# Kernel tuning notes

Measured on AMD Instinct MI355X. Metric: run time of the kernel, lower is better.

## Reference

```python
import jax, jax.numpy as jnp
import numpy as np

N_NODES = 50000
IN_C, HID_C, OUT_C = 128, 128, 64
N_EDGES = 800000


def setup_inputs() -> dict:
    key = jax.random.key(0)
    k1, k2, k3, k4, k5, k6 = jax.random.split(key, 6)
    x = jax.random.normal(k1, (N_NODES, IN_C), dtype=jnp.float32)
    edge_index = jax.random.randint(k2, (2, N_EDGES), 0, N_NODES, dtype=jnp.int64)
    # Glorot-ish init for the two GCN layer weights + biases
    W1 = jax.random.normal(k3, (IN_C, HID_C), dtype=jnp.float32) / np.sqrt(IN_C)
    b1 = jnp.zeros((HID_C,), dtype=jnp.float32)
    W2 = jax.random.normal(k4, (HID_C, OUT_C), dtype=jnp.float32) / np.sqrt(HID_C)
    b2 = jnp.zeros((OUT_C,), dtype=jnp.float32)
    return {"x": x, "edge_index": edge_index, "W1": W1, "b1": b1, "W2": W2, "b2": b2}


def _gcn_norm(edge_index, num_nodes):
    # Add self-loops, then symmetric normalization: deg^-1/2[row] * deg^-1/2[col]
    loops = jnp.arange(num_nodes, dtype=edge_index.dtype)
    row = jnp.concatenate([edge_index[0], loops])  # target nodes
    col = jnp.concatenate([edge_index[1], loops])  # source nodes
    ones = jnp.ones(row.shape[0], dtype=jnp.float32)
    deg = jax.ops.segment_sum(ones, row, num_segments=num_nodes)
    dinv = jnp.where(deg > 0, jax.lax.rsqrt(jnp.maximum(deg, 1.0)), 0.0)
    norm = dinv[row] * dinv[col]  # [E + N]
    return row, col, norm


def _gcn_conv(x, row, col, norm, W, b, num_nodes):
    h = x @ W                              # [N, C_out] — transform first (fewer FLOPs)
    msg = h[col] * norm[:, None]           # gather + scale  [E+N, C_out]
    out = jax.ops.segment_sum(msg, row, num_segments=num_nodes)  # scatter-add
    return out + b


def reference(x, edge_index, W1, b1, W2, b2):
    n = x.shape[0]
    row, col, norm = _gcn_norm(edge_index, n)
    h = _gcn_conv(x, row, col, norm, W1, b1, n)
    # original applies x.relu() then non_linearity (ReLU()) — idempotent, one relu suffices
    h = jax.nn.relu(h)
    return _gcn_conv(h, row, col, norm, W2, b2, n)
```

## Files before the change

### kernel.cpp

```cpp
#include <hip/hip_runtime.h>


#define CHUNKS 256

typedef short bf16x8 __attribute__((ext_vector_type(8)));
typedef float f32x4 __attribute__((ext_vector_type(4)));

__device__ __forceinline__ float bf2f(unsigned int u16) {
    return __uint_as_float(u16 << 16);
}
__device__ __forceinline__ unsigned int f2bf_rne(float f) {
    unsigned int u = __float_as_uint(f);
    return (u + 0x7fffu + ((u >> 16) & 1u)) >> 16;
}
__device__ __forceinline__ unsigned int pack2bf(float a, float b) {
    return f2bf_rne(a) | (f2bf_rne(b) << 16);
}


__global__ __launch_bounds__(256) void hist_kernel(
    const int* __restrict__ row, int E, int CE, int NB, int* __restrict__ cnt)
{
    __shared__ int hist[256];
    const int c = blockIdx.x, t = threadIdx.x;
    hist[t] = 0;
    __syncthreads();
    int s = c * CE, e = min(E, s + CE);
    for (int i = s + t; i < e; i += 256) atomicAdd(&hist[row[i] >> 8], 1);
    __syncthreads();
    if (t < NB) cnt[t * CHUNKS + c] = hist[t];
}

__global__ __launch_bounds__(256) void scanA_kernel(int* __restrict__ cnt, int* __restrict__ tot)
{
    __shared__ int s[256];
    const int b = blockIdx.x, t = threadIdx.x;
    int v = cnt[b * CHUNKS + t];
    s[t] = v; __syncthreads();
    #pragma unroll
    for (int d = 1; d < 256; d <<= 1) {
        int xv = (t >= d) ? s[t - d] : 0;
        __syncthreads();
        s[t] += xv;
        __syncthreads();
    }
    cnt[b * CHUNKS + t] = s[t] - v;
    if (t == 255) tot[b] = s[255];
}

__global__ __launch_bounds__(256) void scanB_kernel(
    const int* __restrict__ tot, int* __restrict__ bstart, int NB, int E)
{
    __shared__ int s[256];
    const int t = threadIdx.x;
    int v = (t < NB) ? tot[t] : 0;
    s[t] = v; __syncthreads();
    #pragma unroll
    for (int d = 1; d < 256; d <<= 1) {
        int xv = (t >= d) ? s[t - d] : 0;
        __syncthreads();
        s[t] += xv;
        __syncthreads();
    }
    if (t < NB) bstart[t] = s[t] - v;
    if (t == 0) bstart[NB] = E;
}

__global__ __launch_bounds__(256) void scatter_kernel(
    const int* __restrict__ row, const int* __restrict__ col, int E, int CE, int NB,
    const int* __restrict__ cnt, const int* __restrict__ bstart,
    unsigned int* __restrict__ bucket)
{
    __shared__ int curL[256];
    const int c = blockIdx.x, t = threadIdx.x;
    if (t < NB) curL[t] = bstart[t] + cnt[t * CHUNKS + c];
    __syncthreads();
    int s = c * CE, e = min(E, s + CE);
    for (int i = s + t; i < e; i += 256) {
        int r = row[i];
        int b = r >> 8;
        int pos = atomicAdd(&curL[b], 1);
        bucket[pos] = (unsigned)(r & 255) | ((unsigned)col[i] << 8);
    }
}

__global__ __launch_bounds__(256) void bucketize_kernel(
    const int* __restrict__ bstart, unsigned int* __restrict__ bucket,
    float* __restrict__ dinv, int2* __restrict__ off2, int N)
{
    __shared__ unsigned int ent[8192];
    __shared__ int hist[256], scn[256], cnt2[256];
    const int b = blockIdx.x, t = threadIdx.x;
    const int n0 = b * 256;

    hist[t] = 0;
    cnt2[t] = 0;
    __syncthreads();

    const int bs = bstart[b], be = bstart[b + 1];
    const int m = min(be - bs, 8192);

    for (int i = t; i < m; i += 256) {
        unsigned int v = bucket[bs + i];
        ent[i] = v;
        atomicAdd(&hist[v & 255u], 1);
    }
    __syncthreads();

    int h = hist[t];
    scn[t] = h;
    __syncthreads();
    #pragma unroll
    for (int d = 1; d < 256; d <<= 1) {
        int xv = (t >= d) ? scn[t - d] : 0;
        __syncthreads();
        scn[t] += xv;
        __syncthreads();
    }
    int base = scn[t] - h;

    int node = n0 + t;
    if (node < N) {
        dinv[node] = rsqrtf((float)(h + 1));
        off2[node] = make_int2(bs + base, bs + base + h);
    }
    scn[t] = base;
    __syncthreads();

    for (int i = t; i < m; i += 256) {
        unsigned int v = ent[i];
        int r = v & 255u;
        int slot = atomicAdd(&cnt2[r], 1);
        bucket[bs + scn[r] + slot] = v >> 8;
    }
}


__global__ __launch_bounds__(256) void wtrans_kernel(
    const float* __restrict__ W, unsigned short* __restrict__ Wt, int C)
{
    int i = blockIdx.x * 256 + threadIdx.x;
    if (i < 128 * C) {
        int k = i / C, c = i - k * C;
        Wt[c * 128 + k] = (unsigned short)f2bf_rne(W[i]);
    }
}

template <int CT>
__global__ __launch_bounds__(256) void gemm_mfma_kernel(
    const float* __restrict__ X, const unsigned short* __restrict__ Wt,
    const float* __restrict__ dinv, unsigned short* __restrict__ out, int N)
{
    constexpr int COUT = CT * 64;
    __shared__ unsigned short As[64 * 128];
    __shared__ unsigned short Bs[COUT * 128];
    __shared__ float dl[64];

    const int t = threadIdx.x;
    const int m0 = blockIdx.x * 64;

    #pragma unroll
    for (int i = 0; i < 8; ++i) {
        int f = i * 256 + t;
        int r = f >> 5, c4 = f & 31;
        int rg = m0 + r;
        float4 v = (rg < N) ? ((const float4*)X)[(size_t)rg * 32 + c4]
                            : make_float4(0.f, 0.f, 0.f, 0.f);
        uint2 p;
        p.x = pack2bf(v.x, v.y);
        p.y = pack2bf(v.z, v.w);
        int cb = c4 * 8;
        *(uint2*)((char*)As + r * 256 + (cb ^ ((r & 7) << 4))) = p;
    }
    #pragma unroll
    for (int i = 0; i < CT * 8; ++i) {
        int f = i * 256 + t;
        int r = f >> 5;
        int cb = (f & 31) * 8;
        uint2 p = ((const uint2*)Wt)[f];
        *(uint2*)((char*)Bs + r * 256 + (cb ^ ((r & 7) << 4))) = p;
    }
    if (t < 64) dl[t] = (m0 + t < N) ? dinv[m0 + t] : 0.f;
    __syncthreads();

    const int w = t >> 6, l = t & 63;
    const int lr = l & 15, lk = l >> 4;

    bf16x8 af[4][4];
    #pragma unroll
    for (int mt = 0; mt < 4; ++mt)
        #pragma unroll
        for (int kt = 0; kt < 4; ++kt) {
            int r = mt * 16 + lr;
            int cb = kt * 64 + lk * 16;
            af[mt][kt] = *(const bf16x8*)((const char*)As + r * 256 + (cb ^ ((r & 7) << 4)));
        }
    bf16x8 bfr[CT][4];
    #pragma unroll
    for (int ct = 0; ct < CT; ++ct)
        #pragma unroll
        for (int kt = 0; kt < 4; ++kt) {
            int c = w * (CT * 16) + ct * 16 + lr;
            int cb = kt * 64 + lk * 16;
            bfr[ct][kt] = *(const bf16x8*)((const char*)Bs + c * 256 + (cb ^ ((c & 7) << 4)));
        }

    f32x4 acc[4][CT];
    #pragma unroll
    for (int mt = 0; mt < 4; ++mt)
        #pragma unroll
        for (int ct = 0; ct < CT; ++ct)
            acc[mt][ct] = f32x4{0.f, 0.f, 0.f, 0.f};

    #pragma unroll
    for (int kt = 0; kt < 4; ++kt)
        #pragma unroll
        for (int mt = 0; mt < 4; ++mt)
            #pragma unroll
            for (int ct = 0; ct < CT; ++ct)
                acc[mt][ct] = __builtin_amdgcn_mfma_f32_16x16x32_bf16(
                    af[mt][kt], bfr[ct][kt], acc[mt][ct], 0, 0, 0);

    #pragma unroll
    for (int mt = 0; mt < 4; ++mt) {
        #pragma unroll
        for (int ct = 0; ct < CT; ++ct) {
            #pragma unroll
            for (int r = 0; r < 4; ++r) {
                int rowl = mt * 16 + lk * 4 + r;
                int grow = m0 + rowl;
                if (grow < N) {
                    int c = w * (CT * 16) + ct * 16 + lr;
                    float v = acc[mt][ct][r] * dl[rowl];
                    out[(size_t)grow * COUT + c] = (unsigned short)f2bf_rne(v);
                }
            }
        }
    }
}


__global__ __launch_bounds__(64) void agg1_kernel(
    const unsigned short* __restrict__ hs, const unsigned int* __restrict__ csr,
    const int2* __restrict__ off2, const float* __restrict__ dinv,
    const float* __restrict__ bias, float* __restrict__ out, int N)
{
    const int n = blockIdx.x;
    const int ch = threadIdx.x * 2;

    unsigned int sv = *(const unsigned int*)&hs[(size_t)n * 128 + ch];
    float ax = bf2f(sv & 0xffffu), ay = bf2f(sv >> 16);

    int2 se = off2[n];
    int j = se.x, e = se.y;
    for (; j + 3 < e; j += 4) {
        int c0 = csr[j], c1 = csr[j + 1], c2 = csr[j + 2], c3 = csr[j + 3];
        unsigned int v0 = *(const unsigned int*)&hs[(size_t)c0 * 128 + ch];
        unsigned int v1 = *(const unsigned int*)&hs[(size_t)c1 * 128 + ch];
        unsigned int v2 = *(const unsigned int*)&hs[(size_t)c2 * 128 + ch];
        unsigned int v3 = *(const unsigned int*)&hs[(size_t)c3 * 128 + ch];
        ax += bf2f(v0 & 0xffffu); ay += bf2f(v0 >> 16);
        ax += bf2f(v1 & 0xffffu); ay += bf2f(v1 >> 16);
        ax += bf2f(v2 & 0xffffu); ay += bf2f(v2 >> 16);
        ax += bf2f(v3 & 0xffffu); ay += bf2f(v3 >> 16);
    }
    for (; j < e; ++j) {
        unsigned int v = *(const unsigned int*)&hs[(size_t)csr[j] * 128 + ch];
        ax += bf2f(v & 0xffffu); ay += bf2f(v >> 16);
    }

    float d = dinv[n];
    float2 b = *(const float2*)&bias[ch];
    float2 o;
    o.x = fmaxf(d * ax + b.x, 0.0f);
    o.y = fmaxf(d * ay + b.y, 0.0f);
    *(float2*)&out[(size_t)n * 128 + ch] = o;
}

__global__ __launch_bounds__(64) void agg2_kernel(
    const unsigned short* __restrict__ hs, const unsigned int* __restrict__ csr,
    const int2* __restrict__ off2, const float* __restrict__ dinv,
    const float* __restrict__ bias, float* __restrict__ out, int N)
{
    const int n = blockIdx.x;
    const int l = threadIdx.x;
    const int half = l >> 5;
    const int ch = (l & 31) * 2;

    int2 se = off2[n];
    int j = se.x, e = se.y;
    float ax = 0.f, ay = 0.f;
    for (; j + 3 < e; j += 4) {
        int c0 = csr[j + half];
        int c1 = csr[j + 2 + half];
        unsigned int v0 = *(const unsigned int*)&hs[(size_t)c0 * 64 + ch];
        unsigned int v1 = *(const unsigned int*)&hs[(size_t)c1 * 64 + ch];
        ax += bf2f(v0 & 0xffffu); ay += bf2f(v0 >> 16);
        ax += bf2f(v1 & 0xffffu); ay += bf2f(v1 >> 16);
    }
    if (j + 1 < e) {
        int c = csr[j + half];
        unsigned int v = *(const unsigned int*)&hs[(size_t)c * 64 + ch];
        ax += bf2f(v & 0xffffu); ay += bf2f(v >> 16);
        j += 2;
    }
    if (j < e && half == 0) {
        unsigned int v = *(const unsigned int*)&hs[(size_t)csr[j] * 64 + ch];
        ax += bf2f(v & 0xffffu); ay += bf2f(v >> 16);
    }

    ax += __shfl_xor(ax, 32);
    ay += __shfl_xor(ay, 32);

    if (half == 0) {
        unsigned int sv = *(const unsigned int*)&hs[(size_t)n * 64 + ch];
        ax += bf2f(sv & 0xffffu); ay += bf2f(sv >> 16);
        float d = dinv[n];
        float2 b = *(const float2*)&bias[ch];
        float2 o;
        o.x = d * ax + b.x;
        o.y = d * ay + b.y;
        *(float2*)&out[(size_t)n * 64 + ch] = o;
    }
}

extern "C" void kernel_launch(void* const* d_in, const int* in_sizes, int n_in,
                              void* d_out, int out_size, void* d_ws, size_t ws_size,
                              hipStream_t stream)
{
    const float* x  = (const float*)d_in[0];
    const int*   ei = (const int*)d_in[1];
    const float* W1 = (const float*)d_in[2];
    const float* b1 = (const float*)d_in[3];
    const float* W2 = (const float*)d_in[4];
    const float* b2 = (const float*)d_in[5];
    float* out = (float*)d_out;

    const int N = in_sizes[0] / 128;
    const int E = in_sizes[1] / 2;
    const int* row = ei;
    const int* col = ei + E;
    const int NB = (N + 255) / 256;
    const int CE = (E + CHUNKS - 1) / CHUNKS;

    char* ws = (char*)d_ws;
    size_t o = 0;
    auto take = [&](size_t bytes) { void* p = ws + o; o = (o + bytes + 255) & ~(size_t)255; return p; };
    int*   cnt    = (int*)  take((size_t)NB * CHUNKS * 4);
    int*   tot    = (int*)  take((size_t)NB * 4);
    int*   bstart = (int*)  take((size_t)(NB + 1) * 4);
    unsigned int* bucket = (unsigned int*)take((size_t)E * 4);
    float* dinv   = (float*)take((size_t)N * 4);
    int2*  off2   = (int2*) take((size_t)N * 8);
    unsigned short* Wt1 = (unsigned short*)take(128 * 128 * 2);
    unsigned short* Wt2 = (unsigned short*)take(64 * 128 * 2);
    unsigned short* hs  = (unsigned short*)take((size_t)N * 128 * 2);
    float* a1     = (float*)take((size_t)N * 128 * 4);
    unsigned short* hs2 = hs;

    hist_kernel<<<CHUNKS, 256, 0, stream>>>(row, E, CE, NB, cnt);
    scanA_kernel<<<NB, 256, 0, stream>>>(cnt, tot);
    scanB_kernel<<<1, 256, 0, stream>>>(tot, bstart, NB, E);
    scatter_kernel<<<CHUNKS, 256, 0, stream>>>(row, col, E, CE, NB, cnt, bstart, bucket);
    bucketize_kernel<<<NB, 256, 0, stream>>>(bstart, bucket, dinv, off2, N);

    wtrans_kernel<<<(128 * 128 + 255) / 256, 256, 0, stream>>>(W1, Wt1, 128);
    wtrans_kernel<<<(128 * 64 + 255) / 256, 256, 0, stream>>>(W2, Wt2, 64);

    gemm_mfma_kernel<2><<<(N + 63) / 64, 256, 0, stream>>>(x, Wt1, dinv, hs, N);
    agg1_kernel<<<N, 64, 0, stream>>>(hs, bucket, off2, dinv, b1, a1, N);

    gemm_mfma_kernel<1><<<(N + 63) / 64, 256, 0, stream>>>(a1, Wt2, dinv, hs2, N);
    agg2_kernel<<<N, 64, 0, stream>>>(hs2, bucket, off2, dinv, b2, out, N);
}
```

Baseline: 123.1 us.

## Store layer-1 activations as bf16 and widen aggregation gathers to 16-byte loads

The first aggregation now writes bf16 activations instead of fp32, which halves the a1 write and the second GEMM's read; the GEMM gains a bf16-input path. Both aggregation kernels now gather 8 channels per lane with uint4 loads and spread neighbors across lane groups, then combine the groups with shuffle reductions. This lowers the number of memory instructions per edge. The two weight-transpose launches are merged into one. The extra bf16 rounding of the intermediate activations changes numerics slightly, though the GEMM already converted that input to bf16.

```diff
diff --git a/kernel.cpp b/kernel.cpp
--- a/kernel.cpp
+++ b/kernel.cpp
@@ -15,6 +15,12 @@
 }
 __device__ __forceinline__ unsigned int pack2bf(float a, float b) {
     return f2bf_rne(a) | (f2bf_rne(b) << 16);
+}
+__device__ __forceinline__ void add8(float* acc, uint4 p) {
+    acc[0] += bf2f(p.x & 0xffffu); acc[1] += bf2f(p.x >> 16);
+    acc[2] += bf2f(p.y & 0xffffu); acc[3] += bf2f(p.y >> 16);
+    acc[4] += bf2f(p.z & 0xffffu); acc[5] += bf2f(p.z >> 16);
+    acc[6] += bf2f(p.w & 0xffffu); acc[7] += bf2f(p.w >> 16);
 }
 
 
@@ -137,18 +143,25 @@
 
 
 __global__ __launch_bounds__(256) void wtrans_kernel(
-    const float* __restrict__ W, unsigned short* __restrict__ Wt, int C)
+    const float* __restrict__ W1, const float* __restrict__ W2,
+    unsigned short* __restrict__ Wt1, unsigned short* __restrict__ Wt2)
 {
     int i = blockIdx.x * 256 + threadIdx.x;
-    if (i < 128 * C) {
-        int k = i / C, c = i - k * C;
-        Wt[c * 128 + k] = (unsigned short)f2bf_rne(W[i]);
-    }
-}
-
-template <int CT>
+    if (i < 128 * 128) {
+        int k = i >> 7, c = i & 127;
+        Wt1[c * 128 + k] = (unsigned short)f2bf_rne(W1[i]);
+    } else {
+        int j = i - 128 * 128;
+        if (j < 128 * 64) {
+            int k = j >> 6, c = j & 63;
+            Wt2[c * 128 + k] = (unsigned short)f2bf_rne(W2[j]);
+        }
+    }
+}
+
+template <int CT, bool BF16IN>
 __global__ __launch_bounds__(256) void gemm_mfma_kernel(
-    const float* __restrict__ X, const unsigned short* __restrict__ Wt,
+    const void* __restrict__ Xv, const unsigned short* __restrict__ Wt,
     const float* __restrict__ dinv, unsigned short* __restrict__ out, int N)
 {
     constexpr int COUT = CT * 64;
@@ -159,18 +172,33 @@
     const int t = threadIdx.x;
     const int m0 = blockIdx.x * 64;
 
-    #pragma unroll
-    for (int i = 0; i < 8; ++i) {
-        int f = i * 256 + t;
-        int r = f >> 5, c4 = f & 31;
-        int rg = m0 + r;
-        float4 v = (rg < N) ? ((const float4*)X)[(size_t)rg * 32 + c4]
-                            : make_float4(0.f, 0.f, 0.f, 0.f);
-        uint2 p;
-        p.x = pack2bf(v.x, v.y);
-        p.y = pack2bf(v.z, v.w);
-        int cb = c4 * 8;
-        *(uint2*)((char*)As + r * 256 + (cb ^ ((r & 7) << 4))) = p;
+    if (BF16IN) {
+        const unsigned short* X = (const unsigned short*)Xv;
+        #pragma unroll
+        for (int i = 0; i < 4; ++i) {
+            int f = i * 256 + t;
+            int r = f >> 4, c16 = f & 15;
+            int rg = m0 + r;
+            uint4 p = (rg < N) ? ((const uint4*)X)[(size_t)rg * 16 + c16]
+                               : make_uint4(0u, 0u, 0u, 0u);
+            int cb = c16 * 16;
+            *(uint4*)((char*)As + r * 256 + (cb ^ ((r & 7) << 4))) = p;
+        }
+    } else {
+        const float* X = (const float*)Xv;
+        #pragma unroll
+        for (int i = 0; i < 8; ++i) {
+            int f = i * 256 + t;
+            int r = f >> 5, c4 = f & 31;
+            int rg = m0 + r;
+            float4 v = (rg < N) ? ((const float4*)X)[(size_t)rg * 32 + c4]
+                                : make_float4(0.f, 0.f, 0.f, 0.f);
+            uint2 p;
+            p.x = pack2bf(v.x, v.y);
+            p.y = pack2bf(v.z, v.w);
+            int cb = c4 * 8;
+            *(uint2*)((char*)As + r * 256 + (cb ^ ((r & 7) << 4))) = p;
+        }
     }
     #pragma unroll
     for (int i = 0; i < CT * 8; ++i) {
@@ -243,38 +271,51 @@
 __global__ __launch_bounds__(64) void agg1_kernel(
     const unsigned short* __restrict__ hs, const unsigned int* __restrict__ csr,
     const int2* __restrict__ off2, const float* __restrict__ dinv,
-    const float* __restrict__ bias, float* __restrict__ out, int N)
+    const float* __restrict__ bias, unsigned short* __restrict__ out, int N)
 {
     const int n = blockIdx.x;
-    const int ch = threadIdx.x * 2;
-
-    unsigned int sv = *(const unsigned int*)&hs[(size_t)n * 128 + ch];
-    float ax = bf2f(sv & 0xffffu), ay = bf2f(sv >> 16);
+    const int l = threadIdx.x;
+    const int q = l & 15, g = l >> 4;
+
+    float acc[8] = {};
+    if (g == 0)
+        add8(acc, *(const uint4*)&hs[(size_t)n * 128 + q * 8]);
 
     int2 se = off2[n];
     int j = se.x, e = se.y;
-    for (; j + 3 < e; j += 4) {
-        int c0 = csr[j], c1 = csr[j + 1], c2 = csr[j + 2], c3 = csr[j + 3];
-        unsigned int v0 = *(const unsigned int*)&hs[(size_t)c0 * 128 + ch];
-        unsigned int v1 = *(const unsigned int*)&hs[(size_t)c1 * 128 + ch];
-        unsigned int v2 = *(const unsigned int*)&hs[(size_t)c2 * 128 + ch];
-        unsigned int v3 = *(const unsigned int*)&hs[(size_t)c3 * 128 + ch];
-        ax += bf2f(v0 & 0xffffu); ay += bf2f(v0 >> 16);
-        ax += bf2f(v1 & 0xffffu); ay += bf2f(v1 >> 16);
-        ax += bf2f(v2 & 0xffffu); ay += bf2f(v2 >> 16);
-        ax += bf2f(v3 & 0xffffu); ay += bf2f(v3 >> 16);
-    }
-    for (; j < e; ++j) {
-        unsigned int v = *(const unsigned int*)&hs[(size_t)csr[j] * 128 + ch];
-        ax += bf2f(v & 0xffffu); ay += bf2f(v >> 16);
-    }
-
-    float d = dinv[n];
-    float2 b = *(const float2*)&bias[ch];
-    float2 o;
-    o.x = fmaxf(d * ax + b.x, 0.0f);
-    o.y = fmaxf(d * ay + b.y, 0.0f);
-    *(float2*)&out[(size_t)n * 128 + ch] = o;
+    for (; j + 7 < e; j += 8) {
+        int c0 = csr[j + g], c1 = csr[j + 4 + g];
+        uint4 p0 = *(const uint4*)&hs[(size_t)c0 * 128 + q * 8];
+        uint4 p1 = *(const uint4*)&hs[(size_t)c1 * 128 + q * 8];
+        add8(acc, p0);
+        add8(acc, p1);
+    }
+    if (j + 3 < e) {
+        add8(acc, *(const uint4*)&hs[(size_t)csr[j + g] * 128 + q * 8]);
+        j += 4;
+    }
+    if (g < e - j)
+        add8(acc, *(const uint4*)&hs[(size_t)csr[j + g] * 128 + q * 8]);
+
+    #pragma unroll
+    for (int i = 0; i < 8; ++i) {
+        acc[i] += __shfl_xor(acc[i], 16);
+        acc[i] += __shfl_xor(acc[i], 32);
+    }
+
+    if (g == 0) {
+        float d = dinv[n];
+        float4 b0 = ((const float4*)bias)[q * 2];
+        float4 b1 = ((const float4*)bias)[q * 2 + 1];
+        float v0 = fmaxf(d * acc[0] + b0.x, 0.f), v1 = fmaxf(d * acc[1] + b0.y, 0.f);
+        float v2 = fmaxf(d * acc[2] + b0.z, 0.f), v3 = fmaxf(d * acc[3] + b0.w, 0.f);
+        float v4 = fmaxf(d * acc[4] + b1.x, 0.f), v5 = fmaxf(d * acc[5] + b1.y, 0.f);
+        float v6 = fmaxf(d * acc[6] + b1.z, 0.f), v7 = fmaxf(d * acc[7] + b1.w, 0.f);
+        uint4 o;
+        o.x = pack2bf(v0, v1); o.y = pack2bf(v2, v3);
+        o.z = pack2bf(v4, v5); o.w = pack2bf(v6, v7);
+        *(uint4*)&out[(size_t)n * 128 + q * 8] = o;
+    }
 }
 
 __global__ __launch_bounds__(64) void agg2_kernel(
@@ -284,43 +325,46 @@
 {
     const int n = blockIdx.x;
     const int l = threadIdx.x;
-    const int half = l >> 5;
-    const int ch = (l & 31) * 2;
+    const int q = l & 7, g = l >> 3;
+
+    float acc[8] = {};
+    if (g == 0)
+        add8(acc, *(const uint4*)&hs[(size_t)n * 64 + q * 8]);
 
     int2 se = off2[n];
     int j = se.x, e = se.y;
-    float ax = 0.f, ay = 0.f;
-    for (; j + 3 < e; j += 4) {
-        int c0 = csr[j + half];
-        int c1 = csr[j + 2 + half];
-        unsigned int v0 = *(const unsigned int*)&hs[(size_t)c0 * 64 + ch];
-        unsigned int v1 = *(const unsigned int*)&hs[(size_t)c1 * 64 + ch];
-        ax += bf2f(v0 & 0xffffu); ay += bf2f(v0 >> 16);
-        ax += bf2f(v1 & 0xffffu); ay += bf2f(v1 >> 16);
-    }
-    if (j + 1 < e) {
-        int c = csr[j + half];
-        unsigned int v = *(const unsigned int*)&hs[(size_t)c * 64 + ch];
-        ax += bf2f(v & 0xffffu); ay += bf2f(v >> 16);
-        j += 2;
-    }
-    if (j < e && half == 0) {
-        unsigned int v = *(const unsigned int*)&hs[(size_t)csr[j] * 64 + ch];
-        ax += bf2f(v & 0xffffu); ay += bf2f(v >> 16);
-    }
-
-    ax += __shfl_xor(ax, 32);
-    ay += __shfl_xor(ay, 32);
-
-    if (half == 0) {
-        unsigned int sv = *(const unsigned int*)&hs[(size_t)n * 64 + ch];
-        ax += bf2f(sv & 0xffffu); ay += bf2f(sv >> 16);
+    for (; j + 15 < e; j += 16) {
+        int c0 = csr[j + g], c1 = csr[j + 8 + g];
+        uint4 p0 = *(const uint4*)&hs[(size_t)c0 * 64 + q * 8];
+        uint4 p1 = *(const uint4*)&hs[(size_t)c1 * 64 + q * 8];
+        add8(acc, p0);
+        add8(acc, p1);
+    }
+    if (j + 7 < e) {
+        add8(acc, *(const uint4*)&hs[(size_t)csr[j + g] * 64 + q * 8]);
+        j += 8;
+    }
+    if (g < e - j)
+        add8(acc, *(const uint4*)&hs[(size_t)csr[j + g] * 64 + q * 8]);
+
+    #pragma unroll
+    for (int i = 0; i < 8; ++i) {
+        acc[i] += __shfl_xor(acc[i], 8);
+        acc[i] += __shfl_xor(acc[i], 16);
+        acc[i] += __shfl_xor(acc[i], 32);
+    }
+
+    if (g == 0) {
         float d = dinv[n];
-        float2 b = *(const float2*)&bias[ch];
-        float2 o;
-        o.x = d * ax + b.x;
-        o.y = d * ay + b.y;
-        *(float2*)&out[(size_t)n * 64 + ch] = o;
+        float4 b0 = ((const float4*)bias)[q * 2];
+        float4 b1 = ((const float4*)bias)[q * 2 + 1];
+        float4 o0, o1;
+        o0.x = d * acc[0] + b0.x; o0.y = d * acc[1] + b0.y;
+        o0.z = d * acc[2] + b0.z; o0.w = d * acc[3] + b0.w;
+        o1.x = d * acc[4] + b1.x; o1.y = d * acc[5] + b1.y;
+        o1.z = d * acc[6] + b1.z; o1.w = d * acc[7] + b1.w;
+        *(float4*)&out[(size_t)n * 64 + q * 8] = o0;
+        *(float4*)&out[(size_t)n * 64 + q * 8 + 4] = o1;
     }
 }
 
@@ -355,7 +399,7 @@
     unsigned short* Wt1 = (unsigned short*)take(128 * 128 * 2);
     unsigned short* Wt2 = (unsigned short*)take(64 * 128 * 2);
     unsigned short* hs  = (unsigned short*)take((size_t)N * 128 * 2);
-    float* a1     = (float*)take((size_t)N * 128 * 4);
+    unsigned short* a1  = (unsigned short*)take((size_t)N * 128 * 2);
     unsigned short* hs2 = hs;
 
     hist_kernel<<<CHUNKS, 256, 0, stream>>>(row, E, CE, NB, cnt);
@@ -364,12 +408,11 @@
     scatter_kernel<<<CHUNKS, 256, 0, stream>>>(row, col, E, CE, NB, cnt, bstart, bucket);
     bucketize_kernel<<<NB, 256, 0, stream>>>(bstart, bucket, dinv, off2, N);
 
-    wtrans_kernel<<<(128 * 128 + 255) / 256, 256, 0, stream>>>(W1, Wt1, 128);
-    wtrans_kernel<<<(128 * 64 + 255) / 256, 256, 0, stream>>>(W2, Wt2, 64);
-
-    gemm_mfma_kernel<2><<<(N + 63) / 64, 256, 0, stream>>>(x, Wt1, dinv, hs, N);
+    wtrans_kernel<<<(128 * 128 + 128 * 64 + 255) / 256, 256, 0, stream>>>(W1, W2, Wt1, Wt2);
+
+    gemm_mfma_kernel<2, false><<<(N + 63) / 64, 256, 0, stream>>>(x, Wt1, dinv, hs, N);
     agg1_kernel<<<N, 64, 0, stream>>>(hs, bucket, off2, dinv, b1, a1, N);
 
-    gemm_mfma_kernel<1><<<(N + 63) / 64, 256, 0, stream>>>(a1, Wt2, dinv, hs2, N);
+    gemm_mfma_kernel<1, true><<<(N + 63) / 64, 256, 0, stream>>>(a1, Wt2, dinv, hs2, N);
     agg2_kernel<<<N, 64, 0, stream>>>(hs2, bucket, off2, dinv, b2, out, N);
 }
```

New measurement: 114.1 us. -7.3%, faster.
